# Kernel optimization log

Measured on AMD Instinct MI355X. Metric: run time of the kernel, lower is better.

Reference implementation:

```python
import jax, jax.numpy as jnp
import numpy as np


def setup_inputs() -> dict:
    key = jax.random.key(0)
    k1, k2, k3 = jax.random.split(key, 3)
    B, F, D = 1024, 784, 512
    x = jax.random.normal(k1, (B, F), dtype=jnp.float32)
    # keras 'uniform' initializer ~ U(-0.05, 0.05)
    Wmin = jax.random.uniform(k2, (D, F), dtype=jnp.float32, minval=-0.05, maxval=0.05)
    Wmax = jax.random.uniform(k3, (D, F), dtype=jnp.float32, minval=-0.05, maxval=0.05)
    return {"x": x, "Wmin": Wmin, "Wmax": Wmax}


def reference(x, Wmin, Wmax):
    # x: [B, F]; Wmin, Wmax: [D, F]
    # L1[b,d] = min_f (x[b,f] - Wmin[d,f]); L2[b,d] = min_f (Wmax[d,f] - x[b,f])
    L1 = jnp.min(x[:, None, :] - Wmin[None, :, :], axis=2)  # [B, D]
    L2 = jnp.min(Wmax[None, :, :] - x[:, None, :], axis=2)  # [B, D]
    # activation is None (linear) in this config
    return jnp.minimum(L1, L2)  # [B, D]
```

## Files before the change

### kernel.cpp

```cpp
#include <hip/hip_runtime.h>


constexpr int F_DIM = 784;
constexpr int BM = 64;
constexpr int BN = 32;
constexpr int BK = 16;
constexpr int LSTR = BK + 4;
constexpr int NCHUNK = F_DIM / BK;
constexpr int ZSPLIT = 7;

typedef float f4v __attribute__((ext_vector_type(4)));
typedef float f2v __attribute__((ext_vector_type(2)));

__global__ __launch_bounds__(256, 4)
void dendral_init_kernel(float* __restrict__ out) {
  const int i = blockIdx.x * 256 + threadIdx.x;
  const float inf = __builtin_inff();
  f4v v = {inf, inf, inf, inf};
  ((f4v*)out)[i] = v;
}

__device__ inline void atomic_min_float(float* addr, float v) {
  if (v >= 0.0f) atomicMin((int*)addr, __float_as_int(v));
  else           atomicMax((unsigned int*)addr, __float_as_uint(v));
}

__global__ __launch_bounds__(256, 4)
void dendral_min_kernel(const float* __restrict__ x,
                        const float* __restrict__ wmin,
                        const float* __restrict__ wmax,
                        float* __restrict__ out, int D) {
  __shared__ float lx[BM * LSTR];
  __shared__ float lwn[BN * LSTR];
  __shared__ float lwx[BN * LSTR];

  const int t  = threadIdx.x;
  const int tx = t & 15;
  const int ty = t >> 4;
  const int b0 = blockIdx.x * BM;
  const int d0 = blockIdx.y * BN;
  const int c0 = blockIdx.z * (NCHUNK / ZSPLIT);
  const int c1 = c0 + (NCHUNK / ZSPLIT);

  const int xr = t >> 2;
  const int xc = (t & 3) << 2;
  const int wt = t >> 7;
  const int wr = (t & 127) >> 2;
  const int wc = (t & 3) << 2;

  const float* xg = x + (size_t)(b0 + xr) * F_DIM + xc;
  const float* wg = (wt ? wmax : wmin) + (size_t)(d0 + wr) * F_DIM + wc;
  float* lds_x = lx + xr * LSTR + xc;
  float* lds_w = (wt ? lwx : lwn) + wr * LSTR + wc;

  f4v px = *(const f4v*)(xg + c0 * BK);
  f4v pw = *(const f4v*)(wg + c0 * BK);

  float l1[4][2], mx[4][2];
#pragma unroll
  for (int r = 0; r < 4; ++r)
#pragma unroll
    for (int c = 0; c < 2; ++c) {
      l1[r][c] = __builtin_inff();
      mx[r][c] = -__builtin_inff();
    }

  for (int kc = c0; kc < c1; ++kc) {
    *(f4v*)lds_x = px;
    *(f4v*)lds_w = pw;
    __syncthreads();
    if (kc + 1 < c1) {
      px = *(const f4v*)(xg + (kc + 1) * BK);
      pw = *(const f4v*)(wg + (kc + 1) * BK);
    }
#pragma unroll
    for (int f = 0; f < BK; f += 4) {
      f4v xv[4], nv[2], wv[2];
#pragma unroll
      for (int r = 0; r < 4; ++r)
        xv[r] = *(const f4v*)&lx[(ty + 16 * r) * LSTR + f];
#pragma unroll
      for (int c = 0; c < 2; ++c) {
        nv[c] = *(const f4v*)&lwn[(tx + 16 * c) * LSTR + f];
        wv[c] = *(const f4v*)&lwx[(tx + 16 * c) * LSTR + f];
      }
#pragma unroll
      for (int r = 0; r < 4; ++r)
#pragma unroll
        for (int c = 0; c < 2; ++c) {
          f2v a_lo = xv[r].xy - nv[c].xy;
          f2v a_hi = xv[r].zw - nv[c].zw;
          l1[r][c] = fminf(l1[r][c], fminf(a_lo.x, a_lo.y));
          l1[r][c] = fminf(l1[r][c], fminf(a_hi.x, a_hi.y));
          f2v u_lo = xv[r].xy - wv[c].xy;
          f2v u_hi = xv[r].zw - wv[c].zw;
          mx[r][c] = fmaxf(mx[r][c], fmaxf(u_lo.x, u_lo.y));
          mx[r][c] = fmaxf(mx[r][c], fmaxf(u_hi.x, u_hi.y));
        }
    }
    __syncthreads();
  }

#pragma unroll
  for (int r = 0; r < 4; ++r)
#pragma unroll
    for (int c = 0; c < 2; ++c) {
      const int b = b0 + ty + 16 * r;
      const int d = d0 + tx + 16 * c;
      atomic_min_float(&out[(size_t)b * D + d], fminf(l1[r][c], -mx[r][c]));
    }
}

extern "C" void kernel_launch(void* const* d_in, const int* in_sizes, int n_in,
                              void* d_out, int out_size, void* d_ws, size_t ws_size,
                              hipStream_t stream) {
  const float* x    = (const float*)d_in[0];
  const float* wmin = (const float*)d_in[1];
  const float* wmax = (const float*)d_in[2];
  float* out = (float*)d_out;
  const int B = in_sizes[0] / F_DIM;
  const int D = in_sizes[1] / F_DIM;

  dendral_init_kernel<<<out_size / (256 * 4), 256, 0, stream>>>(out);

  dim3 grid(B / BM, D / BN, ZSPLIT);
  dendral_min_kernel<<<grid, 256, 0, stream>>>(x, wmin, wmax, out, D);
  (void)n_in; (void)d_ws; (void)ws_size;
}
```

Before: 93.24 us.

## Enlarge block tile to 128x64 with 8x4 register micro-tile and rebalance split-K

Doubles the block tile in both B and D, so each thread now holds an 8x4 micro-tile instead of 4x2, which cuts LDS reads per arithmetic operation. The K split rises from 7 to 12 with uneven chunk boundaries, and each thread now loads all three operands itself. The min and max passes are split into two sub-phases so register pressure stays lower. The cost is more registers (launch bounds lowered to 3 blocks), fewer blocks (8x8x12), and more atomics per output element.

```diff
diff --git a/kernel.cpp b/kernel.cpp
--- a/kernel.cpp
+++ b/kernel.cpp
@@ -2,12 +2,12 @@
 
 
 constexpr int F_DIM = 784;
-constexpr int BM = 64;
-constexpr int BN = 32;
+constexpr int BM = 128;
+constexpr int BN = 64;
 constexpr int BK = 16;
 constexpr int LSTR = BK + 4;
 constexpr int NCHUNK = F_DIM / BK;
-constexpr int ZSPLIT = 7;
+constexpr int ZSPLIT = 12;
 
 typedef float f4v __attribute__((ext_vector_type(4)));
 typedef float f2v __attribute__((ext_vector_type(2)));
@@ -25,7 +25,7 @@
   else           atomicMax((unsigned int*)addr, __float_as_uint(v));
 }
 
-__global__ __launch_bounds__(256, 4)
+__global__ __launch_bounds__(256, 3)
 void dendral_min_kernel(const float* __restrict__ x,
                         const float* __restrict__ wmin,
                         const float* __restrict__ wmax,
@@ -39,72 +39,92 @@
   const int ty = t >> 4;
   const int b0 = blockIdx.x * BM;
   const int d0 = blockIdx.y * BN;
-  const int c0 = blockIdx.z * (NCHUNK / ZSPLIT);
-  const int c1 = c0 + (NCHUNK / ZSPLIT);
+  const int c0 = (blockIdx.z * NCHUNK) / ZSPLIT;
+  const int c1 = ((blockIdx.z + 1) * NCHUNK) / ZSPLIT;
 
-  const int xr = t >> 2;
-  const int xc = (t & 3) << 2;
-  const int wt = t >> 7;
-  const int wr = (t & 127) >> 2;
+  const int xr = t >> 1;
+  const int xc = (t & 1) << 3;
+  const int wr = t >> 2;
   const int wc = (t & 3) << 2;
 
   const float* xg = x + (size_t)(b0 + xr) * F_DIM + xc;
-  const float* wg = (wt ? wmax : wmin) + (size_t)(d0 + wr) * F_DIM + wc;
-  float* lds_x = lx + xr * LSTR + xc;
-  float* lds_w = (wt ? lwx : lwn) + wr * LSTR + wc;
+  const float* ng = wmin + (size_t)(d0 + wr) * F_DIM + wc;
+  const float* wg = wmax + (size_t)(d0 + wr) * F_DIM + wc;
+  float* sx = lx + xr * LSTR + xc;
+  float* sn = lwn + wr * LSTR + wc;
+  float* sw = lwx + wr * LSTR + wc;
 
-  f4v px = *(const f4v*)(xg + c0 * BK);
-  f4v pw = *(const f4v*)(wg + c0 * BK);
+  f4v pxa = *(const f4v*)(xg + c0 * BK);
+  f4v pxb = *(const f4v*)(xg + c0 * BK + 4);
+  f4v pn  = *(const f4v*)(ng + c0 * BK);
+  f4v pw  = *(const f4v*)(wg + c0 * BK);
 
-  float l1[4][2], mx[4][2];
+  float l1[8][4], mx[8][4];
 #pragma unroll
-  for (int r = 0; r < 4; ++r)
+  for (int r = 0; r < 8; ++r)
 #pragma unroll
-    for (int c = 0; c < 2; ++c) {
+    for (int c = 0; c < 4; ++c) {
       l1[r][c] = __builtin_inff();
       mx[r][c] = -__builtin_inff();
     }
 
   for (int kc = c0; kc < c1; ++kc) {
-    *(f4v*)lds_x = px;
-    *(f4v*)lds_w = pw;
+    *(f4v*)sx       = pxa;
+    *(f4v*)(sx + 4) = pxb;
+    *(f4v*)sn       = pn;
+    *(f4v*)sw       = pw;
     __syncthreads();
     if (kc + 1 < c1) {
-      px = *(const f4v*)(xg + (kc + 1) * BK);
-      pw = *(const f4v*)(wg + (kc + 1) * BK);
+      pxa = *(const f4v*)(xg + (kc + 1) * BK);
+      pxb = *(const f4v*)(xg + (kc + 1) * BK + 4);
+      pn  = *(const f4v*)(ng + (kc + 1) * BK);
+      pw  = *(const f4v*)(wg + (kc + 1) * BK);
     }
 #pragma unroll
     for (int f = 0; f < BK; f += 4) {
-      f4v xv[4], nv[2], wv[2];
+      f4v xv[8];
 #pragma unroll
-      for (int r = 0; r < 4; ++r)
+      for (int r = 0; r < 8; ++r)
         xv[r] = *(const f4v*)&lx[(ty + 16 * r) * LSTR + f];
+
+      {
+        f4v nv[4];
 #pragma unroll
-      for (int c = 0; c < 2; ++c) {
-        nv[c] = *(const f4v*)&lwn[(tx + 16 * c) * LSTR + f];
-        wv[c] = *(const f4v*)&lwx[(tx + 16 * c) * LSTR + f];
+        for (int c = 0; c < 4; ++c)
+          nv[c] = *(const f4v*)&lwn[(tx + 16 * c) * LSTR + f];
+#pragma unroll
+        for (int r = 0; r < 8; ++r)
+#pragma unroll
+          for (int c = 0; c < 4; ++c) {
+            f2v a_lo = xv[r].xy - nv[c].xy;
+            f2v a_hi = xv[r].zw - nv[c].zw;
+            l1[r][c] = fminf(l1[r][c], fminf(a_lo.x, a_lo.y));
+            l1[r][c] = fminf(l1[r][c], fminf(a_hi.x, a_hi.y));
+          }
       }
+      {
+        f4v wv[4];
 #pragma unroll
-      for (int r = 0; r < 4; ++r)
+        for (int c = 0; c < 4; ++c)
+          wv[c] = *(const f4v*)&lwx[(tx + 16 * c) * LSTR + f];
 #pragma unroll
-        for (int c = 0; c < 2; ++c) {
-          f2v a_lo = xv[r].xy - nv[c].xy;
-          f2v a_hi = xv[r].zw - nv[c].zw;
-          l1[r][c] = fminf(l1[r][c], fminf(a_lo.x, a_lo.y));
-          l1[r][c] = fminf(l1[r][c], fminf(a_hi.x, a_hi.y));
-          f2v u_lo = xv[r].xy - wv[c].xy;
-          f2v u_hi = xv[r].zw - wv[c].zw;
-          mx[r][c] = fmaxf(mx[r][c], fmaxf(u_lo.x, u_lo.y));
-          mx[r][c] = fmaxf(mx[r][c], fmaxf(u_hi.x, u_hi.y));
-        }
+        for (int r = 0; r < 8; ++r)
+#pragma unroll
+          for (int c = 0; c < 4; ++c) {
+            f2v u_lo = xv[r].xy - wv[c].xy;
+            f2v u_hi = xv[r].zw - wv[c].zw;
+            mx[r][c] = fmaxf(mx[r][c], fmaxf(u_lo.x, u_lo.y));
+            mx[r][c] = fmaxf(mx[r][c], fmaxf(u_hi.x, u_hi.y));
+          }
+      }
     }
     __syncthreads();
   }
 
 #pragma unroll
-  for (int r = 0; r < 4; ++r)
+  for (int r = 0; r < 8; ++r)
 #pragma unroll
-    for (int c = 0; c < 2; ++c) {
+    for (int c = 0; c < 4; ++c) {
       const int b = b0 + ty + 16 * r;
       const int d = d0 + tx + 16 * c;
       atomic_min_float(&out[(size_t)b * D + d], fminf(l1[r][c], -mx[r][c]));
```

Result: slower. 112.8 us (+21.0%).

## Drop LDS staging, read operands directly from global, replace atomics with workspace reduction

Applied to the files above, without the earlier changes.

The main kernel no longer stages x and weight tiles through shared memory with barriers. Each thread now loads float4 vectors straight from global memory, relying on the cache, and computes twice as many rows per thread (BM 128, 8x2 accumulators). The split-K partial results go to per-slice workspace buffers, and a separate reduce kernel combines them, replacing the init kernel and the float atomic-min. This removes LDS traffic, barriers and atomic contention, at the cost of redundant global/L1 loads, higher register pressure, and extra workspace write/read traffic. There is also a fallback that uses zsplit=1 when the workspace is too small.

```diff
diff --git a/kernel.cpp b/kernel.cpp
--- a/kernel.cpp
+++ b/kernel.cpp
@@ -2,90 +2,63 @@
 
 
 constexpr int F_DIM = 784;
-constexpr int BM = 64;
+constexpr int NQ = F_DIM / 4;
+constexpr int BM = 128;
 constexpr int BN = 32;
-constexpr int BK = 16;
-constexpr int LSTR = BK + 4;
-constexpr int NCHUNK = F_DIM / BK;
 constexpr int ZSPLIT = 7;
 
 typedef float f4v __attribute__((ext_vector_type(4)));
 typedef float f2v __attribute__((ext_vector_type(2)));
 
-__global__ __launch_bounds__(256, 4)
-void dendral_init_kernel(float* __restrict__ out) {
-  const int i = blockIdx.x * 256 + threadIdx.x;
-  const float inf = __builtin_inff();
-  f4v v = {inf, inf, inf, inf};
-  ((f4v*)out)[i] = v;
-}
-
-__device__ inline void atomic_min_float(float* addr, float v) {
-  if (v >= 0.0f) atomicMin((int*)addr, __float_as_int(v));
-  else           atomicMax((unsigned int*)addr, __float_as_uint(v));
-}
-
-__global__ __launch_bounds__(256, 4)
-void dendral_min_kernel(const float* __restrict__ x,
-                        const float* __restrict__ wmin,
-                        const float* __restrict__ wmax,
-                        float* __restrict__ out, int D) {
-  __shared__ float lx[BM * LSTR];
-  __shared__ float lwn[BN * LSTR];
-  __shared__ float lwx[BN * LSTR];
-
+__global__ __launch_bounds__(256, 3)
+void dendral_main(const float* __restrict__ x,
+                  const float* __restrict__ wmin,
+                  const float* __restrict__ wmax,
+                  float* __restrict__ dst,
+                  int D, long long sliceN, int zsplit) {
   const int t  = threadIdx.x;
   const int tx = t & 15;
   const int ty = t >> 4;
   const int b0 = blockIdx.x * BM;
   const int d0 = blockIdx.y * BN;
-  const int c0 = blockIdx.z * (NCHUNK / ZSPLIT);
-  const int c1 = c0 + (NCHUNK / ZSPLIT);
+  const int z  = blockIdx.z;
+  const int q0 = (z * NQ) / zsplit;
+  const int q1 = ((z + 1) * NQ) / zsplit;
 
-  const int xr = t >> 2;
-  const int xc = (t & 3) << 2;
-  const int wt = t >> 7;
-  const int wr = (t & 127) >> 2;
-  const int wc = (t & 3) << 2;
+  const float* xr[8];
+#pragma unroll
+  for (int r = 0; r < 8; ++r)
+    xr[r] = x + (size_t)(b0 + ty + 16 * r) * F_DIM;
+  const float* nr[2]; const float* wr[2];
+#pragma unroll
+  for (int c = 0; c < 2; ++c) {
+    nr[c] = wmin + (size_t)(d0 + tx + 16 * c) * F_DIM;
+    wr[c] = wmax + (size_t)(d0 + tx + 16 * c) * F_DIM;
+  }
 
-  const float* xg = x + (size_t)(b0 + xr) * F_DIM + xc;
-  const float* wg = (wt ? wmax : wmin) + (size_t)(d0 + wr) * F_DIM + wc;
-  float* lds_x = lx + xr * LSTR + xc;
-  float* lds_w = (wt ? lwx : lwn) + wr * LSTR + wc;
-
-  f4v px = *(const f4v*)(xg + c0 * BK);
-  f4v pw = *(const f4v*)(wg + c0 * BK);
-
-  float l1[4][2], mx[4][2];
+  float l1[8][2], mx[8][2];
 #pragma unroll
-  for (int r = 0; r < 4; ++r)
+  for (int r = 0; r < 8; ++r)
 #pragma unroll
     for (int c = 0; c < 2; ++c) {
       l1[r][c] = __builtin_inff();
       mx[r][c] = -__builtin_inff();
     }
 
-  for (int kc = c0; kc < c1; ++kc) {
-    *(f4v*)lds_x = px;
-    *(f4v*)lds_w = pw;
-    __syncthreads();
-    if (kc + 1 < c1) {
-      px = *(const f4v*)(xg + (kc + 1) * BK);
-      pw = *(const f4v*)(wg + (kc + 1) * BK);
-    }
+  for (int q = q0; q < q1; q += 4) {
 #pragma unroll
-    for (int f = 0; f < BK; f += 4) {
-      f4v xv[4], nv[2], wv[2];
+    for (int k = 0; k < 4; ++k) {
+      f4v xv[8], nv[2], wv[2];
 #pragma unroll
-      for (int r = 0; r < 4; ++r)
-        xv[r] = *(const f4v*)&lx[(ty + 16 * r) * LSTR + f];
+      for (int r = 0; r < 8; ++r)
+        xv[r] = *(const f4v*)(xr[r] + (q + k) * 4);
 #pragma unroll
       for (int c = 0; c < 2; ++c) {
-        nv[c] = *(const f4v*)&lwn[(tx + 16 * c) * LSTR + f];
-        wv[c] = *(const f4v*)&lwx[(tx + 16 * c) * LSTR + f];
+        nv[c] = *(const f4v*)(nr[c] + (q + k) * 4);
+        wv[c] = *(const f4v*)(wr[c] + (q + k) * 4);
       }
 #pragma unroll
-      for (int r = 0; r < 4; ++r)
+      for (int r = 0; r < 8; ++r)
 #pragma unroll
         for (int c = 0; c < 2; ++c) {
           f2v a_lo = xv[r].xy - nv[c].xy;
@@ -98,17 +71,30 @@
           mx[r][c] = fmaxf(mx[r][c], fmaxf(u_hi.x, u_hi.y));
         }
     }
-    __syncthreads();
   }
 
+  float* o = dst + (size_t)z * sliceN;
 #pragma unroll
-  for (int r = 0; r < 4; ++r)
+  for (int r = 0; r < 8; ++r)
 #pragma unroll
     for (int c = 0; c < 2; ++c) {
       const int b = b0 + ty + 16 * r;
       const int d = d0 + tx + 16 * c;
-      atomic_min_float(&out[(size_t)b * D + d], fminf(l1[r][c], -mx[r][c]));
+      o[(size_t)b * D + d] = fminf(l1[r][c], -mx[r][c]);
     }
+}
+
+__global__ __launch_bounds__(256, 4)
+void dendral_reduce(const float* __restrict__ ws, float* __restrict__ out,
+                    long long sliceN, int zsplit) {
+  const long long i = (long long)blockIdx.x * 256 + threadIdx.x;
+  f4v m = ((const f4v*)ws)[i];
+  for (int z = 1; z < zsplit; ++z) {
+    f4v v = ((const f4v*)(ws + (size_t)z * sliceN))[i];
+    m.x = fminf(m.x, v.x); m.y = fminf(m.y, v.y);
+    m.z = fminf(m.z, v.z); m.w = fminf(m.w, v.w);
+  }
+  ((f4v*)out)[i] = m;
 }
 
 extern "C" void kernel_launch(void* const* d_in, const int* in_sizes, int n_in,
@@ -120,10 +106,18 @@
   float* out = (float*)d_out;
   const int B = in_sizes[0] / F_DIM;
   const int D = in_sizes[1] / F_DIM;
+  const long long sliceN = (long long)B * D;
 
-  dendral_init_kernel<<<out_size / (256 * 4), 256, 0, stream>>>(out);
+  const int zsplit = (ws_size >= (size_t)ZSPLIT * sliceN * sizeof(float))
+                         ? ZSPLIT : 1;
+  float* dst = (zsplit > 1) ? (float*)d_ws : out;
 
-  dim3 grid(B / BM, D / BN, ZSPLIT);
-  dendral_min_kernel<<<grid, 256, 0, stream>>>(x, wmin, wmax, out, D);
-  (void)n_in; (void)d_ws; (void)ws_size;
+  dim3 grid(B / BM, D / BN, zsplit);
+  dendral_main<<<grid, 256, 0, stream>>>(x, wmin, wmax, dst, D, sliceN, zsplit);
+
+  if (zsplit > 1) {
+    dendral_reduce<<<(int)(sliceN / (256 * 4)), 256, 0, stream>>>(
+        (const float*)d_ws, out, sliceN, zsplit);
+  }
+  (void)n_in; (void)out_size;
 }
```

Measured after the change: 331.8 us. 3.56x slower.
